# Kernel optimization log

Measured on AMD Instinct MI355X. Metric: run time of the kernel, lower is better.

The kernel has to match this reference:

```python
import jax, jax.numpy as jnp
import numpy as np

B, S, D, H, DK, DV, DFF, L, V = 8, 1024, 256, 8, 32, 32, 1024, 4, 28
EPS = 1e-5
NEG = -1e9


def _ln(x, w, b):
    m = jnp.mean(x, axis=-1, keepdims=True)
    v = jnp.var(x, axis=-1, keepdims=True)
    return (x - m) * jax.lax.rsqrt(v + EPS) * w + b


def setup_inputs() -> dict:
    key = jax.random.key(0)
    ks = jax.random.split(key, 30)
    std = 0.02
    inp = {
        'input_ids': jax.random.randint(ks[0], (B, S), 0, V),
        'tok_embed': jax.random.normal(ks[1], (V, D), jnp.float32) * std,
        'pos_embed': jax.random.normal(ks[2], (S, D), jnp.float32) * std,
        'emb_ln_w': jnp.ones((D,), jnp.float32),
        'emb_ln_b': jnp.zeros((D,), jnp.float32),
        'Wq': jax.random.normal(ks[3], (L, D, H * DK), jnp.float32) * std,
        'bq': jnp.zeros((L, H * DK), jnp.float32),
        'Wk': jax.random.normal(ks[4], (L, D, H * DK), jnp.float32) * std,
        'bk': jnp.zeros((L, H * DK), jnp.float32),
        'Wv': jax.random.normal(ks[5], (L, D, H * DV), jnp.float32) * std,
        'bv': jnp.zeros((L, H * DV), jnp.float32),
        'Wo': jax.random.normal(ks[6], (L, H * DV, D), jnp.float32) * std,
        'bo': jnp.zeros((L, D), jnp.float32),
        'ln_w': jnp.ones((L, D), jnp.float32),
        'ln_b': jnp.zeros((L, D), jnp.float32),
        'W1': jax.random.normal(ks[7], (L, D, DFF), jnp.float32) * std,
        'b1': jnp.zeros((L, DFF), jnp.float32),
        'W2': jax.random.normal(ks[8], (L, DFF, D), jnp.float32) * std,
        'b2': jnp.zeros((L, D), jnp.float32),
        'ft1_w': jax.random.normal(ks[9], (D, D), jnp.float32) * std,
        'ft1_b': jnp.zeros((D,), jnp.float32),
        'ft2_w': jax.random.normal(ks[10], (D, D // 2), jnp.float32) * std,
        'ft2_b': jnp.zeros((D // 2,), jnp.float32),
        'cls_w': jax.random.normal(ks[11], (D // 2, 2), jnp.float32) * std,
        'cls_b': jnp.zeros((2,), jnp.float32),
    }
    return inp


def reference(input_ids, tok_embed, pos_embed, emb_ln_w, emb_ln_b,
              Wq, bq, Wk, bk, Wv, bv, Wo, bo, ln_w, ln_b,
              W1, b1, W2, b2, ft1_w, ft1_b, ft2_w, ft2_b, cls_w, cls_b):
    # Embedding: tok + pos, then LayerNorm
    x = tok_embed[input_ids] + pos_embed[jnp.arange(S)][None, :, :]
    x = _ln(x, emb_ln_w, emb_ln_b)
    # pad mask: True where key position is pad (token id 0); broadcast [B,1,1,S]
    pad = (input_ids == 0)[:, None, None, :]
    scale = 1.0 / np.sqrt(DK)
    for i in range(L):
        residual = x
        q = (x @ Wq[i] + bq[i]).reshape(B, S, H, DK).transpose(0, 2, 1, 3)
        k = (x @ Wk[i] + bk[i]).reshape(B, S, H, DK).transpose(0, 2, 1, 3)
        v = (x @ Wv[i] + bv[i]).reshape(B, S, H, DV).transpose(0, 2, 1, 3)
        scores = jnp.einsum('bhqd,bhkd->bhqk', q, k) * scale
        scores = jnp.where(pad, NEG, scores)
        attn = jax.nn.softmax(scores, axis=-1)
        ctx = jnp.einsum('bhqk,bhkd->bhqd', attn, v)
        ctx = ctx.transpose(0, 2, 1, 3).reshape(B, S, H * DV)
        x = _ln(ctx @ Wo[i] + bo[i] + residual, ln_w[i], ln_b[i])
        # FFN (note: original has NO residual/norm after FFN)
        x = jax.nn.relu(x @ W1[i] + b1[i]) @ W2[i] + b2[i]
    cls = x[:, 0, :]
    feat = jax.nn.relu(cls @ ft1_w + ft1_b) @ ft2_w + ft2_b  # dropout = eval no-op
    logits = feat @ cls_w + cls_b
    return logits, feat
```

## Files before the change

kernel.cpp:

```cpp
#include <hip/hip_runtime.h>
#include <math.h>

#define S_ 1024
#define D_ 256

typedef __attribute__((ext_vector_type(8))) _Float16 half8;
typedef __attribute__((ext_vector_type(4))) _Float16 half4;
typedef __attribute__((ext_vector_type(2))) _Float16 half2v;
typedef __attribute__((ext_vector_type(4))) float f32x4;
typedef __attribute__((ext_vector_type(4))) unsigned int u32x4;

__device__ __forceinline__ float wave_sum64(float x) {
    x += __shfl_xor(x, 32); x += __shfl_xor(x, 16); x += __shfl_xor(x, 8);
    x += __shfl_xor(x, 4);  x += __shfl_xor(x, 2);  x += __shfl_xor(x, 1);
    return x;
}

#define GLD16(gp, lp) __builtin_amdgcn_global_load_lds( \
    (const __attribute__((address_space(1))) void*)(gp), \
    (__attribute__((address_space(3))) void*)(lp), 16, 0, 0)

__global__ __launch_bounds__(256) void transpose_cvt(
    const float* __restrict__ src, _Float16* __restrict__ dst, int K, int N)
{
    __shared__ float tile[32][33];
    src += (size_t)blockIdx.z * K * N;
    dst += (size_t)blockIdx.z * K * N;
    const int bx = blockIdx.x * 32;
    const int by = blockIdx.y * 32;
    const int t = threadIdx.x;
    const int c = t & 31, r0 = t >> 5;
    #pragma unroll
    for (int j = 0; j < 4; ++j)
        tile[r0 + 8 * j][c] = src[(size_t)(by + r0 + 8 * j) * N + bx + c];
    __syncthreads();
    #pragma unroll
    for (int j = 0; j < 4; ++j)
        dst[(size_t)(bx + r0 + 8 * j) * K + by + c] = (_Float16)tile[c][r0 + 8 * j];
}

__global__ __launch_bounds__(256) void transpose_qkv(
    const float* __restrict__ Wq, const float* __restrict__ Wk,
    const float* __restrict__ Wv, _Float16* __restrict__ qkvT)
{
    __shared__ float tile[32][33];
    const int z = blockIdx.z, l = z / 3, m = z % 3;
    const float* src = (m == 0 ? Wq : (m == 1 ? Wk : Wv)) + (size_t)l * 65536;
    _Float16* dst = qkvT + (size_t)l * 196608 + (size_t)m * 65536;
    const int bx = blockIdx.x * 32;
    const int by = blockIdx.y * 32;
    const int t = threadIdx.x;
    const int c = t & 31, r0 = t >> 5;
    #pragma unroll
    for (int j = 0; j < 4; ++j)
        tile[r0 + 8 * j][c] = src[(size_t)(by + r0 + 8 * j) * 256 + bx + c];
    __syncthreads();
    #pragma unroll
    for (int j = 0; j < 4; ++j)
        dst[(size_t)(bx + r0 + 8 * j) * 256 + by + c] = (_Float16)tile[c][r0 + 8 * j];
}

__global__ __launch_bounds__(256) void pack_bias(
    const float* __restrict__ bq, const float* __restrict__ bk,
    const float* __restrict__ bv, float* __restrict__ bqkv)
{
    const int z = blockIdx.x, l = z / 3, m = z % 3;
    const float* s = (m == 0 ? bq : (m == 1 ? bk : bv)) + l * 256;
    bqkv[l * 768 + m * 256 + threadIdx.x] = s[threadIdx.x];
}

__global__ __launch_bounds__(256) void embed_ln_kernel(
    const int* __restrict__ ids, const float* __restrict__ tok,
    const float* __restrict__ pos, const float* __restrict__ w,
    const float* __restrict__ b, float* __restrict__ X, _Float16* __restrict__ Xh)
{
    const int wv_ = threadIdx.x >> 6, lane = threadIdx.x & 63;
    const int tokid = blockIdx.x * 4 + wv_;
    const int s = tokid & (S_ - 1);
    const int id = ids[tokid];
    float4 e = *(const float4*)&tok[id * D_ + lane * 4];
    float4 p = *(const float4*)&pos[s * D_ + lane * 4];
    float4 x = make_float4(e.x + p.x, e.y + p.y, e.z + p.z, e.w + p.w);
    float sum = x.x + x.y + x.z + x.w;
    float sq  = x.x * x.x + x.y * x.y + x.z * x.z + x.w * x.w;
    sum = wave_sum64(sum); sq = wave_sum64(sq);
    float mean = sum * (1.f / D_);
    float var  = sq * (1.f / D_) - mean * mean;
    float rs   = rsqrtf(var + 1e-5f);
    float4 wv = *(const float4*)&w[lane * 4];
    float4 bv = *(const float4*)&b[lane * 4];
    float4 o = make_float4((x.x - mean) * rs * wv.x + bv.x,
                           (x.y - mean) * rs * wv.y + bv.y,
                           (x.z - mean) * rs * wv.z + bv.z,
                           (x.w - mean) * rs * wv.w + bv.w);
    *(float4*)&X[(size_t)tokid * D_ + lane * 4] = o;
    half4 oh = { (_Float16)o.x, (_Float16)o.y, (_Float16)o.z, (_Float16)o.w };
    *(half4*)&Xh[(size_t)tokid * D_ + lane * 4] = oh;
}

__global__ __launch_bounds__(256) void ln_kernel(
    const float* __restrict__ Y, const float* __restrict__ w,
    const float* __restrict__ b, _Float16* __restrict__ Th)
{
    const int wv_ = threadIdx.x >> 6, lane = threadIdx.x & 63;
    const int tokid = blockIdx.x * 4 + wv_;
    const size_t base = (size_t)tokid * D_ + lane * 4;
    float4 x = *(const float4*)&Y[base];
    float sum = x.x + x.y + x.z + x.w;
    float sq  = x.x * x.x + x.y * x.y + x.z * x.z + x.w * x.w;
    sum = wave_sum64(sum); sq = wave_sum64(sq);
    float mean = sum * (1.f / D_);
    float var  = sq * (1.f / D_) - mean * mean;
    float rs   = rsqrtf(var + 1e-5f);
    float4 wv = *(const float4*)&w[lane * 4];
    float4 bv = *(const float4*)&b[lane * 4];
    half4 oh = { (_Float16)((x.x - mean) * rs * wv.x + bv.x),
                 (_Float16)((x.y - mean) * rs * wv.y + bv.y),
                 (_Float16)((x.z - mean) * rs * wv.z + bv.z),
                 (_Float16)((x.w - mean) * rs * wv.w + bv.w) };
    *(half4*)&Th[base] = oh;
}

template<int MODE>
__global__ __launch_bounds__(256) void gemm_f16(
    const _Float16* __restrict__ A, const _Float16* __restrict__ Bt,
    const float* __restrict__ bias, const float* __restrict__ res,
    float* __restrict__ Cf, _Float16* __restrict__ Ch,
    int K, int N)
{
    __shared__ _Float16 As[2][8192];
    const int t = threadIdx.x;
    const int wid = t >> 6, lane = t & 63;
    const int wr = wid >> 1, wc = wid & 1;
    const int m0 = blockIdx.x * 128, n0 = blockIdx.y * 64;
    const int li = lane & 15, lg = lane >> 4;
    const int srow = lane >> 3;
    const int scg = (lane & 7) ^ srow;

    f32x4 acc[4][2];
    const f32x4 zf = {0.f, 0.f, 0.f, 0.f};
    #pragma unroll
    for (int mr = 0; mr < 4; ++mr) { acc[mr][0] = zf; acc[mr][1] = zf; }

    const int KT = K >> 6;
    {
        const _Float16* Ab = A + (size_t)m0 * K;
        #pragma unroll
        for (int j = 0; j < 4; ++j) {
            int row = (wid * 4 + j) * 8 + srow;
            GLD16(Ab + (size_t)row * K + scg * 8, &As[0][(wid * 4 + j) * 512]);
        }
    }

    for (int kt = 0; kt < KT; ++kt) {
        const int cur = kt & 1;
        half8 bfr[2][2];
        #pragma unroll
        for (int nr = 0; nr < 2; ++nr) {
            const _Float16* bp = Bt + (size_t)(n0 + wc * 32 + nr * 16 + li) * K + kt * 64 + lg * 8;
            bfr[nr][0] = *(const half8*)bp;
            bfr[nr][1] = *(const half8*)(bp + 32);
        }
        if (kt + 1 < KT) {
            const _Float16* Ab = A + (size_t)m0 * K + (kt + 1) * 64;
            #pragma unroll
            for (int j = 0; j < 4; ++j) {
                int row = (wid * 4 + j) * 8 + srow;
                GLD16(Ab + (size_t)row * K + scg * 8, &As[cur ^ 1][(wid * 4 + j) * 512]);
            }
            asm volatile("s_waitcnt vmcnt(8)" ::: "memory");
        } else {
            asm volatile("s_waitcnt vmcnt(4)" ::: "memory");
        }
        __builtin_amdgcn_s_barrier();
        #pragma unroll
        for (int kk = 0; kk < 2; ++kk) {
            half8 af[4];
            #pragma unroll
            for (int mr = 0; mr < 4; ++mr) {
                int arow = wr * 64 + mr * 16 + li;
                int ablk = (kk * 4 + lg) ^ (li & 7);
                af[mr] = *(const half8*)&As[cur][arow * 64 + ablk * 8];
            }
            #pragma unroll
            for (int mr = 0; mr < 4; ++mr)
                #pragma unroll
                for (int nr = 0; nr < 2; ++nr)
                    acc[mr][nr] = __builtin_amdgcn_mfma_f32_16x16x32_f16(
                        af[mr], bfr[nr][kk], acc[mr][nr], 0, 0, 0);
        }
        __builtin_amdgcn_s_barrier();
    }

    #pragma unroll
    for (int nr = 0; nr < 2; ++nr) {
        const int n = n0 + wc * 32 + nr * 16 + li;
        const float bv = bias[n];
        #pragma unroll
        for (int mr = 0; mr < 4; ++mr) {
            #pragma unroll
            for (int r = 0; r < 4; ++r) {
                const int m = m0 + wr * 64 + mr * 16 + lg * 4 + r;
                float o = acc[mr][nr][r] + bv;
                if (MODE == 1) o = fmaxf(o, 0.f);
                if (MODE == 4) o += res[(size_t)m * N + n];
                if (MODE == 0 || MODE == 2 || MODE == 4) Cf[(size_t)m * N + n] = o;
                if (MODE == 1 || MODE == 2 || MODE == 3) Ch[(size_t)m * N + n] = (_Float16)o;
            }
        }
    }
}

template<int MODE>
__global__ __launch_bounds__(256) void gemm64_f16(
    const _Float16* __restrict__ A, const _Float16* __restrict__ Bt,
    const float* __restrict__ bias, const float* __restrict__ res,
    float* __restrict__ Cf, _Float16* __restrict__ Ch,
    int K, int N)
{
    __shared__ _Float16 As[2][4096];
    const int t = threadIdx.x;
    const int wid = t >> 6, lane = t & 63;
    const int wr = wid >> 1, wc = wid & 1;
    const int m0 = blockIdx.x * 64, n0 = blockIdx.y * 64;
    const int li = lane & 15, lg = lane >> 4;
    const int srow = lane >> 3;
    const int scg = (lane & 7) ^ srow;

    f32x4 acc[2][2];
    const f32x4 zf = {0.f, 0.f, 0.f, 0.f};
    acc[0][0] = zf; acc[0][1] = zf; acc[1][0] = zf; acc[1][1] = zf;

    const int KT = K >> 6;
    {
        const _Float16* Ab = A + (size_t)m0 * K;
        #pragma unroll
        for (int j = 0; j < 2; ++j) {
            int rb = j * 32 + wid * 8;
            GLD16(Ab + (size_t)(rb + srow) * K + scg * 8, &As[0][rb * 64]);
        }
    }

    for (int kt = 0; kt < KT; ++kt) {
        const int cur = kt & 1;
        half8 bfr[2][2];
        #pragma unroll
        for (int nr = 0; nr < 2; ++nr) {
            const _Float16* bp = Bt + (size_t)(n0 + wc * 32 + nr * 16 + li) * K + kt * 64 + lg * 8;
            bfr[nr][0] = *(const half8*)bp;
            bfr[nr][1] = *(const half8*)(bp + 32);
        }
        if (kt + 1 < KT) {
            const _Float16* Ab = A + (size_t)m0 * K + (kt + 1) * 64;
            #pragma unroll
            for (int j = 0; j < 2; ++j) {
                int rb = j * 32 + wid * 8;
                GLD16(Ab + (size_t)(rb + srow) * K + scg * 8, &As[cur ^ 1][rb * 64]);
            }
            asm volatile("s_waitcnt vmcnt(6)" ::: "memory");
        } else {
            asm volatile("s_waitcnt vmcnt(4)" ::: "memory");
        }
        __builtin_amdgcn_s_barrier();
        #pragma unroll
        for (int kk = 0; kk < 2; ++kk) {
            half8 af[2];
            #pragma unroll
            for (int mr = 0; mr < 2; ++mr) {
                int arow = wr * 32 + mr * 16 + li;
                int ablk = (kk * 4 + lg) ^ (li & 7);
                af[mr] = *(const half8*)&As[cur][arow * 64 + ablk * 8];
            }
            #pragma unroll
            for (int mr = 0; mr < 2; ++mr)
                #pragma unroll
                for (int nr = 0; nr < 2; ++nr)
                    acc[mr][nr] = __builtin_amdgcn_mfma_f32_16x16x32_f16(
                        af[mr], bfr[nr][kk], acc[mr][nr], 0, 0, 0);
        }
        __builtin_amdgcn_s_barrier();
    }

    #pragma unroll
    for (int nr = 0; nr < 2; ++nr) {
        const int n = n0 + wc * 32 + nr * 16 + li;
        const float bv = bias[n];
        #pragma unroll
        for (int mr = 0; mr < 2; ++mr) {
            #pragma unroll
            for (int r = 0; r < 4; ++r) {
                const int m = m0 + wr * 32 + mr * 16 + lg * 4 + r;
                float o = acc[mr][nr][r] + bv;
                if (MODE == 1) o = fmaxf(o, 0.f);
                if (MODE == 4) o += res[(size_t)m * N + n];
                if (MODE == 0 || MODE == 2 || MODE == 4) Cf[(size_t)m * N + n] = o;
                if (MODE == 1 || MODE == 2 || MODE == 3) Ch[(size_t)m * N + n] = (_Float16)o;
            }
        }
    }
}

__global__ __launch_bounds__(256, 4) void attn_f16_kernel(
    const _Float16* __restrict__ qkv, const int* __restrict__ ids,
    _Float16* __restrict__ ctxo)
{
    __shared__ unsigned int VTp[2][32 * 38];
    __shared__ float maskn[2][64];
    const int t = threadIdx.x;
    const int bh = blockIdx.x, b = bh >> 3, h = bh & 7;
    const int q0 = blockIdx.y * 64;
    const int wid = t >> 6;
    const int lane = t & 63;
    const int i = lane & 15;
    const int g = lane >> 4;
    const int kp = t >> 3;
    const int v0s = (t & 7) * 4;

    const size_t bS = (size_t)b * S_;
    const float scale = 0.17677669529663687f * 1.4426950408889634f;

    const half8 qf = *(const half8*)(qkv + (bS + q0 + wid * 16 + i) * 768 + h * 32 + g * 8);

    float l = 0.f;
    f32x4 cacc[2];
    const f32x4 zf = {0.f, 0.f, 0.f, 0.f};
    cacc[0] = zf; cacc[1] = zf;

    const _Float16* kbase = qkv + 256 + (bS + i) * 768 + h * 32 + g * 8;
    const _Float16* vbase = qkv + 512 + (bS + 2 * kp) * 768 + h * 32 + v0s;

    {
        const ushort* vb = (const ushort*)vbase;
        ushort4 a0 = *(const ushort4*)vb;
        ushort4 a1 = *(const ushort4*)(vb + 768);
        VTp[0][(v0s + 0) * 38 + kp] = (unsigned)a0.x | ((unsigned)a1.x << 16);
        VTp[0][(v0s + 1) * 38 + kp] = (unsigned)a0.y | ((unsigned)a1.y << 16);
        VTp[0][(v0s + 2) * 38 + kp] = (unsigned)a0.z | ((unsigned)a1.z << 16);
        VTp[0][(v0s + 3) * 38 + kp] = (unsigned)a0.w | ((unsigned)a1.w << 16);
        if (t < 64) maskn[0][t] = (ids[bS + t] == 0) ? -1e9f : 0.f;
    }
    f32x4 sc[4];
    #pragma unroll
    for (int c = 0; c < 4; ++c)
        sc[c] = __builtin_amdgcn_mfma_f32_16x16x32_f16(
            *(const half8*)(kbase + c * 16 * 768), qf, zf, 0, 0, 0);

    for (int kt = 0; kt < 16; ++kt) {
        const int cur = kt & 1;
        __syncthreads();
        ushort4 a0, a1;
        int midv = 1;
        half8 kf[4];
        const bool have = (kt < 15);
        if (have) {
            const ushort* vb = (const ushort*)(vbase + (size_t)(kt + 1) * 64 * 768);
            a0 = *(const ushort4*)vb;
            a1 = *(const ushort4*)(vb + 768);
            if (t < 64) midv = ids[bS + (kt + 1) * 64 + t];
            const _Float16* kb = kbase + (size_t)(kt + 1) * 64 * 768;
            #pragma unroll
            for (int c = 0; c < 4; ++c) kf[c] = *(const half8*)(kb + c * 16 * 768);
        }
        float p[4][4];
        float psum = 0.f;
        #pragma unroll
        for (int c = 0; c < 4; ++c) {
            float4 ad = *(const float4*)&maskn[cur][c * 16 + g * 4];
            p[c][0] = exp2f(fmaf(sc[c][0], scale, ad.x));
            p[c][1] = exp2f(fmaf(sc[c][1], scale, ad.y));
            p[c][2] = exp2f(fmaf(sc[c][2], scale, ad.z));
            p[c][3] = exp2f(fmaf(sc[c][3], scale, ad.w));
            psum += (p[c][0] + p[c][1]) + (p[c][2] + p[c][3]);
        }
        l += psum;
        if (have) {
            #pragma unroll
            for (int c = 0; c < 4; ++c)
                sc[c] = __builtin_amdgcn_mfma_f32_16x16x32_f16(kf[c], qf, zf, 0, 0, 0);
        }
        if (have) {
            VTp[cur ^ 1][(v0s + 0) * 38 + kp] = (unsigned)a0.x | ((unsigned)a1.x << 16);
            VTp[cur ^ 1][(v0s + 1) * 38 + kp] = (unsigned)a0.y | ((unsigned)a1.y << 16);
            VTp[cur ^ 1][(v0s + 2) * 38 + kp] = (unsigned)a0.z | ((unsigned)a1.z << 16);
            VTp[cur ^ 1][(v0s + 3) * 38 + kp] = (unsigned)a0.w | ((unsigned)a1.w << 16);
            if (t < 64) maskn[cur ^ 1][t] = (midv == 0) ? -1e9f : 0.f;
        }
        #pragma unroll
        for (int c = 0; c < 4; ++c) {
            half2v plo = __builtin_bit_cast(half2v, __builtin_amdgcn_cvt_pkrtz(p[c][0], p[c][1]));
            half2v phi = __builtin_bit_cast(half2v, __builtin_amdgcn_cvt_pkrtz(p[c][2], p[c][3]));
            half4 pb = { plo[0], plo[1], phi[0], phi[1] };
            #pragma unroll
            for (int vh = 0; vh < 2; ++vh) {
                const unsigned int* vp = &VTp[cur][(vh * 16 + i) * 38 + 8 * c + 2 * g];
                unsigned long long vv = *(const unsigned long long*)vp;
                half4 vf = __builtin_bit_cast(half4, vv);
                cacc[vh] = __builtin_amdgcn_mfma_f32_16x16x16f16(vf, pb, cacc[vh], 0, 0, 0);
            }
        }
    }
    l += __shfl_xor(l, 16);
    l += __shfl_xor(l, 32);
    const float inv = 1.f / l;
    _Float16* crow = ctxo + (bS + q0 + wid * 16 + i) * 256 + h * 32;
    #pragma unroll
    for (int vh = 0; vh < 2; ++vh) {
        half4 st;
        #pragma unroll
        for (int r = 0; r < 4; ++r) st[r] = (_Float16)(cacc[vh][r] * inv);
        *(half4*)&crow[vh * 16 + g * 4] = st;
    }
}

__global__ __launch_bounds__(256) void head1_kernel(
    const float* __restrict__ X, const float* __restrict__ ft1w,
    const float* __restrict__ ft1b, float* __restrict__ h1)
{
    __shared__ float clsS[8][256];
    __shared__ float ps[8][8][32];
    const int t = threadIdx.x;
    #pragma unroll
    for (int b = 0; b < 8; ++b) clsS[b][t] = X[(size_t)b * S_ * D_ + t];
    __syncthreads();
    const int n = t & 31, dg = t >> 5;
    const int gn = blockIdx.x * 32 + n;
    float s[8] = {};
    for (int dd = 0; dd < 32; ++dd) {
        int d = dg * 32 + dd;
        float w = ft1w[d * 256 + gn];
        #pragma unroll
        for (int b = 0; b < 8; ++b) s[b] = fmaf(clsS[b][d], w, s[b]);
    }
    #pragma unroll
    for (int b = 0; b < 8; ++b) ps[dg][b][n] = s[b];
    __syncthreads();
    {
        const int b = t >> 5, nn = t & 31;
        float a = 0.f;
        #pragma unroll
        for (int g = 0; g < 8; ++g) a += ps[g][b][nn];
        const int gn2 = blockIdx.x * 32 + nn;
        h1[b * 256 + gn2] = fmaxf(a + ft1b[gn2], 0.f);
    }
}

__global__ __launch_bounds__(256) void head2_kernel(
    const float* __restrict__ h1, const float* __restrict__ ft2w,
    const float* __restrict__ ft2b, float* __restrict__ featW,
    float* __restrict__ out)
{
    __shared__ float hS[8][256];
    __shared__ float ps[8][8][32];
    const int t = threadIdx.x;
    #pragma unroll
    for (int b = 0; b < 8; ++b) hS[b][t] = h1[b * 256 + t];
    __syncthreads();
    const int n = t & 31, dg = t >> 5;
    const int gn = blockIdx.x * 32 + n;
    float s[8] = {};
    for (int dd = 0; dd < 32; ++dd) {
        int d = dg * 32 + dd;
        float w = ft2w[d * 128 + gn];
        #pragma unroll
        for (int b = 0; b < 8; ++b) s[b] = fmaf(hS[b][d], w, s[b]);
    }
    #pragma unroll
    for (int b = 0; b < 8; ++b) ps[dg][b][n] = s[b];
    __syncthreads();
    {
        const int b = t >> 5, nn = t & 31;
        float a = 0.f;
        #pragma unroll
        for (int g = 0; g < 8; ++g) a += ps[g][b][nn];
        const int gn2 = blockIdx.x * 32 + nn;
        float v = a + ft2b[gn2];
        featW[b * 128 + gn2] = v;
        out[16 + b * 128 + gn2] = v;
    }
}

__global__ __launch_bounds__(64) void head3_kernel(
    const float* __restrict__ featW, const float* __restrict__ clw,
    const float* __restrict__ clb, float* __restrict__ out)
{
    const int t = threadIdx.x;
    if (t < 16) {
        const int b = t >> 1, c = t & 1;
        float s = 0.f;
        for (int d = 0; d < 128; ++d) s = fmaf(featW[b * 128 + d], clw[d * 2 + c], s);
        out[t] = s + clb[c];
    }
}

extern "C" void kernel_launch(void* const* d_in, const int* in_sizes, int n_in,
                              void* d_out, int out_size, void* d_ws, size_t ws_size,
                              hipStream_t stream)
{
    const int*   ids  = (const int*)d_in[0];
    const float* tok  = (const float*)d_in[1];
    const float* pos  = (const float*)d_in[2];
    const float* elnw = (const float*)d_in[3];
    const float* elnb = (const float*)d_in[4];
    const float* Wq   = (const float*)d_in[5];
    const float* bq   = (const float*)d_in[6];
    const float* Wk   = (const float*)d_in[7];
    const float* bk   = (const float*)d_in[8];
    const float* Wv   = (const float*)d_in[9];
    const float* bv   = (const float*)d_in[10];
    const float* Wo   = (const float*)d_in[11];
    const float* bo   = (const float*)d_in[12];
    const float* lnw  = (const float*)d_in[13];
    const float* lnb  = (const float*)d_in[14];
    const float* W1   = (const float*)d_in[15];
    const float* b1   = (const float*)d_in[16];
    const float* W2   = (const float*)d_in[17];
    const float* b2   = (const float*)d_in[18];
    const float* ft1w = (const float*)d_in[19];
    const float* ft1b = (const float*)d_in[20];
    const float* ft2w = (const float*)d_in[21];
    const float* ft2b = (const float*)d_in[22];
    const float* clw  = (const float*)d_in[23];
    const float* clb  = (const float*)d_in[24];
    float* out = (float*)d_out;

    char* ws = (char*)d_ws;
    float*    X    = (float*)(ws);
    float*    Y    = (float*)(ws + (8ull << 20));
    _Float16* Xh   = (_Float16*)(ws + (16ull << 20));
    _Float16* Th   = (_Float16*)(ws + (20ull << 20));
    _Float16* qkvb = (_Float16*)(ws + (24ull << 20));
    _Float16* ctx  = (_Float16*)(ws + (36ull << 20));
    _Float16* Hb   = (_Float16*)(ws + (24ull << 20));
    _Float16* qkvT = (_Float16*)(ws + (40ull << 20));
    _Float16* WoT  = (_Float16*)(ws + (42ull << 20));
    _Float16* W1T  = (_Float16*)(ws + (43ull << 20));
    _Float16* W2T  = (_Float16*)(ws + (45ull << 20));
    float*    bqkv = (float*)(ws + (47ull << 20));
    float*    h1W  = (float*)(ws + (47ull << 20) + (16ull << 10));
    float*    feW  = (float*)(ws + (47ull << 20) + (24ull << 10));

    transpose_qkv<<<dim3(8, 8, 12), 256, 0, stream>>>(Wq, Wk, Wv, qkvT);
    transpose_cvt<<<dim3(8, 8, 4),  256, 0, stream>>>(Wo, WoT, 256, 256);
    transpose_cvt<<<dim3(32, 8, 4), 256, 0, stream>>>(W1, W1T, 256, 1024);
    transpose_cvt<<<dim3(8, 32, 4), 256, 0, stream>>>(W2, W2T, 1024, 256);
    pack_bias<<<12, 256, 0, stream>>>(bq, bk, bv, bqkv);

    embed_ln_kernel<<<2048, 256, 0, stream>>>(ids, tok, pos, elnw, elnb, X, Xh);

    for (int i = 0; i < 4; ++i) {
        gemm_f16<3><<<dim3(64, 12), 256, 0, stream>>>(
            Xh, qkvT + (size_t)i * 196608, bqkv + i * 768, nullptr, nullptr, qkvb, 256, 768);
        attn_f16_kernel<<<dim3(64, 16), 256, 0, stream>>>(qkvb, ids, ctx);
        gemm64_f16<4><<<dim3(128, 4), 256, 0, stream>>>(
            ctx, WoT + (size_t)i * 65536, bo + i * 256, X, Y, nullptr, 256, 256);
        ln_kernel<<<2048, 256, 0, stream>>>(Y, lnw + i * 256, lnb + i * 256, Th);
        gemm_f16<1><<<dim3(64, 16), 256, 0, stream>>>(
            Th, W1T + (size_t)i * 262144, b1 + i * 1024, nullptr, nullptr, Hb, 256, 1024);
        gemm64_f16<2><<<dim3(128, 4), 256, 0, stream>>>(
            Hb, W2T + (size_t)i * 262144, b2 + i * 256, nullptr, X, Xh, 1024, 256);
    }

    head1_kernel<<<8, 256, 0, stream>>>(X, ft1w, ft1b, h1W);
    head2_kernel<<<4, 256, 0, stream>>>(h1W, ft2w, ft2b, feW, out);
    head3_kernel<<<1, 64, 0, stream>>>(feW, clw, clb, out);
}
```

Measured before the change: 429.3 us.

## Fuse Wo projection, bias, residual and LayerNorm into one kernel

```diff
diff --git a/kernel.cpp b/kernel.cpp
--- a/kernel.cpp
+++ b/kernel.cpp
@@ -98,29 +98,6 @@
     *(half4*)&Xh[(size_t)tokid * D_ + lane * 4] = oh;
 }
 
-__global__ __launch_bounds__(256) void ln_kernel(
-    const float* __restrict__ Y, const float* __restrict__ w,
-    const float* __restrict__ b, _Float16* __restrict__ Th)
-{
-    const int wv_ = threadIdx.x >> 6, lane = threadIdx.x & 63;
-    const int tokid = blockIdx.x * 4 + wv_;
-    const size_t base = (size_t)tokid * D_ + lane * 4;
-    float4 x = *(const float4*)&Y[base];
-    float sum = x.x + x.y + x.z + x.w;
-    float sq  = x.x * x.x + x.y * x.y + x.z * x.z + x.w * x.w;
-    sum = wave_sum64(sum); sq = wave_sum64(sq);
-    float mean = sum * (1.f / D_);
-    float var  = sq * (1.f / D_) - mean * mean;
-    float rs   = rsqrtf(var + 1e-5f);
-    float4 wv = *(const float4*)&w[lane * 4];
-    float4 bv = *(const float4*)&b[lane * 4];
-    half4 oh = { (_Float16)((x.x - mean) * rs * wv.x + bv.x),
-                 (_Float16)((x.y - mean) * rs * wv.y + bv.y),
-                 (_Float16)((x.z - mean) * rs * wv.z + bv.z),
-                 (_Float16)((x.w - mean) * rs * wv.w + bv.w) };
-    *(half4*)&Th[base] = oh;
-}
-
 template<int MODE>
 __global__ __launch_bounds__(256) void gemm_f16(
     const _Float16* __restrict__ A, const _Float16* __restrict__ Bt,
@@ -297,6 +274,92 @@
                 if (MODE == 1 || MODE == 2 || MODE == 3) Ch[(size_t)m * N + n] = (_Float16)o;
             }
         }
+    }
+}
+
+__global__ __launch_bounds__(256) void gemm_wo_ln(
+    const _Float16* __restrict__ A,
+    const _Float16* __restrict__ Bt,
+    const float* __restrict__ bias, const float* __restrict__ res,
+    const float* __restrict__ lnw, const float* __restrict__ lnb,
+    _Float16* __restrict__ Th)
+{
+    __shared__ float tile[16][260];
+    const int t = threadIdx.x;
+    const int wid = t >> 6, lane = t & 63;
+    const int li = lane & 15, lg = lane >> 4;
+    const int m0 = blockIdx.x * 16;
+
+    f32x4 acc[4];
+    const f32x4 zf = {0.f, 0.f, 0.f, 0.f};
+    #pragma unroll
+    for (int nr = 0; nr < 4; ++nr) acc[nr] = zf;
+
+    #pragma unroll
+    for (int kt = 0; kt < 4; ++kt) {
+        const _Float16* ap = A + (size_t)(m0 + li) * 256 + kt * 64 + lg * 8;
+        half8 af0 = *(const half8*)ap;
+        half8 af1 = *(const half8*)(ap + 32);
+        #pragma unroll
+        for (int nr = 0; nr < 4; ++nr) {
+            const _Float16* bp = Bt + (size_t)(wid * 64 + nr * 16 + li) * 256 + kt * 64 + lg * 8;
+            half8 b0 = *(const half8*)bp;
+            half8 b1 = *(const half8*)(bp + 32);
+            acc[nr] = __builtin_amdgcn_mfma_f32_16x16x32_f16(af0, b0, acc[nr], 0, 0, 0);
+            acc[nr] = __builtin_amdgcn_mfma_f32_16x16x32_f16(af1, b1, acc[nr], 0, 0, 0);
+        }
+    }
+    #pragma unroll
+    for (int nr = 0; nr < 4; ++nr)
+        #pragma unroll
+        for (int r = 0; r < 4; ++r)
+            tile[lg * 4 + r][wid * 64 + nr * 16 + li] = acc[nr][r];
+    __syncthreads();
+
+    const int rr = t >> 4, c16 = t & 15;
+    float y[16];
+    float sum = 0.f, sq = 0.f;
+    #pragma unroll
+    for (int j4 = 0; j4 < 4; ++j4) {
+        const int c = c16 * 16 + j4 * 4;
+        float4 rv = *(const float4*)&res[(size_t)(m0 + rr) * 256 + c];
+        float4 bv = *(const float4*)&bias[c];
+        #pragma unroll
+        for (int j = 0; j < 4; ++j) {
+            float bb = (j == 0) ? bv.x : (j == 1) ? bv.y : (j == 2) ? bv.z : bv.w;
+            float rrv = (j == 0) ? rv.x : (j == 1) ? rv.y : (j == 2) ? rv.z : rv.w;
+            float v = tile[rr][c + j] + bb + rrv;
+            y[j4 * 4 + j] = v;
+            sum += v;
+            sq = fmaf(v, v, sq);
+        }
+    }
+    #pragma unroll
+    for (int mk = 1; mk <= 8; mk <<= 1) {
+        sum += __shfl_xor(sum, mk);
+        sq  += __shfl_xor(sq, mk);
+    }
+    const float mean = sum * (1.f / 256.f);
+    const float var  = sq * (1.f / 256.f) - mean * mean;
+    const float rs   = rsqrtf(var + 1e-5f);
+
+    #pragma unroll
+    for (int h8 = 0; h8 < 2; ++h8) {
+        const int c = c16 * 16 + h8 * 8;
+        float4 w0 = *(const float4*)&lnw[c];
+        float4 w1 = *(const float4*)&lnw[c + 4];
+        float4 b0 = *(const float4*)&lnb[c];
+        float4 b1 = *(const float4*)&lnb[c + 4];
+        half8 o;
+        o[0] = (_Float16)((y[h8 * 8 + 0] - mean) * rs * w0.x + b0.x);
+        o[1] = (_Float16)((y[h8 * 8 + 1] - mean) * rs * w0.y + b0.y);
+        o[2] = (_Float16)((y[h8 * 8 + 2] - mean) * rs * w0.z + b0.z);
+        o[3] = (_Float16)((y[h8 * 8 + 3] - mean) * rs * w0.w + b0.w);
+        o[4] = (_Float16)((y[h8 * 8 + 4] - mean) * rs * w1.x + b1.x);
+        o[5] = (_Float16)((y[h8 * 8 + 5] - mean) * rs * w1.y + b1.y);
+        o[6] = (_Float16)((y[h8 * 8 + 6] - mean) * rs * w1.z + b1.z);
+        o[7] = (_Float16)((y[h8 * 8 + 7] - mean) * rs * w1.w + b1.w);
+        *(half8*)&Th[(size_t)(m0 + rr) * 256 + c] = o;
     }
 }
 
@@ -525,7 +588,6 @@
 
     char* ws = (char*)d_ws;
     float*    X    = (float*)(ws);
-    float*    Y    = (float*)(ws + (8ull << 20));
     _Float16* Xh   = (_Float16*)(ws + (16ull << 20));
     _Float16* Th   = (_Float16*)(ws + (20ull << 20));
     _Float16* qkvb = (_Float16*)(ws + (24ull << 20));
@@ -551,9 +613,9 @@
         gemm_f16<3><<<dim3(64, 12), 256, 0, stream>>>(
             Xh, qkvT + (size_t)i * 196608, bqkv + i * 768, nullptr, nullptr, qkvb, 256, 768);
         attn_f16_kernel<<<dim3(64, 16), 256, 0, stream>>>(qkvb, ids, ctx);
-        gemm64_f16<4><<<dim3(128, 4), 256, 0, stream>>>(
-            ctx, WoT + (size_t)i * 65536, bo + i * 256, X, Y, nullptr, 256, 256);
-        ln_kernel<<<2048, 256, 0, stream>>>(Y, lnw + i * 256, lnb + i * 256, Th);
+        gemm_wo_ln<<<512, 256, 0, stream>>>(
+            ctx, WoT + (size_t)i * 65536, bo + i * 256, X,
+            lnw + i * 256, lnb + i * 256, Th);
         gemm_f16<1><<<dim3(64, 16), 256, 0, stream>>>(
             Th, W1T + (size_t)i * 262144, b1 + i * 1024, nullptr, nullptr, Hb, 256, 1024);
         gemm64_f16<2><<<dim3(128, 4), 256, 0, stream>>>(
```

Result: slower. 442.6 us (+3.1%).
